# Optimization experiments

Measured on AMD Instinct MI355X. Metric: run time of the kernel, lower is better.

Reference implementation:

```python
import jax, jax.numpy as jnp
import numpy as np

N = 10000      # nodes
E = 65536      # edges
IN = 16        # in_channels
H = 64         # hidden_channels
ED = 4         # edge_attr_dim
MLP_H = 64     # hidden width of edge-weight MLPs


def _glorot(key, shape):
    fan_in, fan_out = shape[0], shape[1]
    lim = np.sqrt(6.0 / (fan_in + fan_out)).astype(np.float32)
    return jax.random.uniform(key, shape, jnp.float32, -lim, lim)


def setup_inputs() -> dict:
    key = jax.random.key(0)
    ks = jax.random.split(key, 16)
    x = jax.random.normal(ks[0], (N, IN), dtype=jnp.float32)
    edge_index = jax.random.randint(ks[1], (2, E), 0, N, dtype=jnp.int64)
    edge_attr = jax.random.normal(ks[2], (E, ED), dtype=jnp.float32)
    return {
        "x": x,
        "edge_index": edge_index,
        "edge_attr": edge_attr,
        # nn1: Linear(ED,64) -> ReLU -> Linear(64, IN*H)
        "nn1_w1": _glorot(ks[3], (ED, MLP_H)), "nn1_b1": jnp.zeros((MLP_H,), jnp.float32),
        "nn1_w2": _glorot(ks[4], (MLP_H, IN * H)), "nn1_b2": jnp.zeros((IN * H,), jnp.float32),
        "root1": _glorot(ks[5], (IN, H)), "bias1": jnp.zeros((H,), jnp.float32),
        # nn2: Linear(ED,64) -> ReLU -> Linear(64, H*H)
        "nn2_w1": _glorot(ks[6], (ED, MLP_H)), "nn2_b1": jnp.zeros((MLP_H,), jnp.float32),
        "nn2_w2": _glorot(ks[7], (MLP_H, H * H)), "nn2_b2": jnp.zeros((H * H,), jnp.float32),
        "root2": _glorot(ks[8], (H, H)), "bias2": jnp.zeros((H,), jnp.float32),
        # readout MLP
        "lin1_w": _glorot(ks[9], (H, 8)), "lin1_b": jnp.zeros((8,), jnp.float32),
        "lin2_w": _glorot(ks[10], (8, 1)), "lin2_b": jnp.zeros((1,), jnp.float32),
    }


def _nnconv(x, src, dst, edge_attr, w1, b1, w2, b2, root, bias, cin, cout):
    # Edge-conditioned weight generation: MLP(edge_attr) -> [E, cin, cout]
    h = jax.nn.relu(edge_attr @ w1 + b1)
    We = (h @ w2 + b2).reshape(-1, cin, cout)
    # Per-edge matmul: message_e = x[src_e] @ We_e  -> [E, cout]
    msg = jnp.einsum('ei,eio->eo', x[src], We)
    # Scatter mean over destination nodes
    s = jax.ops.segment_sum(msg, dst, num_segments=N)
    cnt = jax.ops.segment_sum(jnp.ones((msg.shape[0],), x.dtype), dst, num_segments=N)
    agg = s / jnp.maximum(cnt, 1.0)[:, None]
    # Root transform + bias (PyG NNConv defaults: root_weight=True, bias=True)
    return agg + x @ root + bias


def reference(x, edge_index, edge_attr,
              nn1_w1, nn1_b1, nn1_w2, nn1_b2, root1, bias1,
              nn2_w1, nn2_b1, nn2_w2, nn2_b2, root2, bias2,
              lin1_w, lin1_b, lin2_w, lin2_b):
    # Dropout layers are identity in eval mode.
    src, dst = edge_index[0], edge_index[1]
    h = jax.nn.relu(_nnconv(x, src, dst, edge_attr,
                            nn1_w1, nn1_b1, nn1_w2, nn1_b2, root1, bias1, IN, H))
    h = jax.nn.relu(_nnconv(h, src, dst, edge_attr,
                            nn2_w1, nn2_b1, nn2_w2, nn2_b2, root2, bias2, H, H))
    h = jax.nn.relu(h @ lin1_w + lin1_b)
    return (h @ lin2_w + lin2_b)[:, 0]  # squeeze(-1) -> [N]
```

## Files before the change

kernel.cpp:

```cpp
#include <hip/hip_runtime.h>
#include <hip/hip_bf16.h>

#define NN 10000
#define EE 65536

using short8  = __attribute__((ext_vector_type(8))) short;
using float4v = __attribute__((ext_vector_type(4))) float;

__device__ __forceinline__ unsigned short f2b(float f){
  union { float f; unsigned int u; } v; v.f = f;
  unsigned int u = v.u;
  unsigned int r = (u + 0x7fff + ((u >> 16) & 1)) >> 16;
  return (unsigned short)r;
}


__global__ void k_hist(const int* __restrict__ dst, int* __restrict__ cnt){
  int e = blockIdx.x*256 + threadIdx.x;
  if(e < EE) atomicAdd(&cnt[dst[e]], 1);
}

__global__ __launch_bounds__(1024) void k_scan(const int* __restrict__ cnt, int* __restrict__ offs, int* __restrict__ cursor){
  const int T = 1024, PER = (NN + T - 1)/T;
  int tid = threadIdx.x;
  int base = tid*PER;
  int local[PER];
  int s = 0;
  #pragma unroll
  for(int j=0;j<PER;j++){
    int i = base+j;
    int v = (i<NN)? cnt[i] : 0;
    local[j] = s;
    s += v;
  }
  int lane = tid & 63, wv = tid >> 6;
  int val = s;
  #pragma unroll
  for(int o=1;o<64;o<<=1){
    int u = __shfl_up(val, o, 64);
    if(lane >= o) val += u;
  }
  __shared__ int wsum[16];
  if(lane==63) wsum[wv] = val;
  __syncthreads();
  if(tid==0){
    int acc=0;
    #pragma unroll
    for(int i=0;i<16;i++){ int t2=wsum[i]; wsum[i]=acc; acc+=t2; }
  }
  __syncthreads();
  int thr_excl = wsum[wv] + (val - s);
  #pragma unroll
  for(int j=0;j<PER;j++){
    int i = base+j;
    if(i<NN){ int e = thr_excl + local[j]; offs[i]=e; cursor[i]=e; }
  }
  if(tid == T-1) offs[NN] = thr_excl + s;
}

__global__ void k_scatter(const int* __restrict__ dst, int* __restrict__ cursor, int* __restrict__ elist){
  int e = blockIdx.x*256 + threadIdx.x;
  if(e < EE){ int p = atomicAdd(&cursor[dst[e]], 1); elist[p] = e; }
}


__global__ void k_permB(const float* __restrict__ w2, unsigned short* __restrict__ Bt, int cin){
  int idx = blockIdx.x*256 + threadIdx.x;
  int K = cin*64;
  int total = 64*K;
  if(idx < total){
    int o = idx / K;
    int k = idx - o*K;
    int m = k / cin;
    int i = k - m*cin;
    Bt[idx] = f2b(w2[(size_t)m*(cin*64) + i*64 + o]);
  }
}


__global__ void k_edge_mlp(const float* __restrict__ ea, const float* __restrict__ w1,
                           const float* __restrict__ b1, float* __restrict__ h){
  int idx = blockIdx.x*256 + threadIdx.x;
  if(idx < EE*64){
    int m = idx & 63;
    int e = idx >> 6;
    const float* a = ea + (size_t)e*4;
    float acc = b1[m] + a[0]*w1[m] + a[1]*w1[64+m] + a[2]*w1[128+m] + a[3]*w1[192+m];
    h[idx] = fmaxf(acc, 0.f);
  }
}


__global__ __launch_bounds__(64) void k_accK1(const float* __restrict__ x, const int* __restrict__ src,
    const int* __restrict__ offs, const int* __restrict__ elist, const float* __restrict__ h,
    unsigned short* __restrict__ K1, float* __restrict__ XS, int v0){
  int v = v0 + blockIdx.x;
  int L = threadIdx.x;
  int i = L & 15, mg = L >> 4;
  __shared__ float sh[2][64];
  float acc[16];
  #pragma unroll
  for(int j=0;j<16;j++) acc[j]=0.f;
  float xs = 0.f;
  int p0 = offs[v], p1 = offs[v+1];
  float h_nxt = 0.f, x_nxt = 0.f;
  if(p0 < p1){
    int e = elist[p0];
    h_nxt = h[(size_t)e*64 + L];
    x_nxt = x[(size_t)src[e]*16 + i];
  }
  for(int p=p0;p<p1;p++){
    int buf = (p-p0)&1;
    float hv = h_nxt, xv = x_nxt;
    sh[buf][L] = hv;
    __syncthreads();
    if(p+1<p1){
      int e = elist[p+1];
      h_nxt = h[(size_t)e*64 + L];
      x_nxt = x[(size_t)src[e]*16 + i];
    }
    xs += xv;
    #pragma unroll
    for(int j4=0;j4<4;j4++){
      float4 h4 = *(float4*)&sh[buf][mg*16 + j4*4];
      acc[j4*4+0] += h4.x*xv; acc[j4*4+1] += h4.y*xv;
      acc[j4*4+2] += h4.z*xv; acc[j4*4+3] += h4.w*xv;
    }
  }
  unsigned short* Kv = K1 + (size_t)blockIdx.x*1024;
  #pragma unroll
  for(int j=0;j<16;j++) Kv[(mg*16+j)*16 + i] = f2b(acc[j]);
  if(mg==0) XS[(size_t)v*64 + i] = xs;
}


__global__ __launch_bounds__(64) void k_accK2(const float* __restrict__ x1, const int* __restrict__ src,
    const int* __restrict__ offs, const int* __restrict__ elist, const float* __restrict__ h,
    unsigned short* __restrict__ K, float* __restrict__ XS, int v0){
  int v = v0 + blockIdx.x;
  int L = threadIdx.x;
  __shared__ float sh[2][64];
  float acc[64];
  #pragma unroll
  for(int m=0;m<64;m++) acc[m]=0.f;
  float xs = 0.f;
  int p0 = offs[v], p1 = offs[v+1];
  float h_nxt = 0.f, x_nxt = 0.f;
  if(p0 < p1){
    int e = elist[p0];
    h_nxt = h[(size_t)e*64 + L];
    x_nxt = x1[(size_t)src[e]*64 + L];
  }
  for(int p=p0;p<p1;p++){
    int buf = (p-p0)&1;
    float hv = h_nxt, xv = x_nxt;
    sh[buf][L] = hv;
    __syncthreads();
    if(p+1<p1){
      int e = elist[p+1];
      h_nxt = h[(size_t)e*64 + L];
      x_nxt = x1[(size_t)src[e]*64 + L];
    }
    xs += xv;
    #pragma unroll
    for(int m4=0;m4<16;m4++){
      float4 h4 = *(float4*)&sh[buf][m4*4];
      acc[m4*4+0] += h4.x*xv; acc[m4*4+1] += h4.y*xv;
      acc[m4*4+2] += h4.z*xv; acc[m4*4+3] += h4.w*xv;
    }
  }
  unsigned short* Kv = K + (size_t)blockIdx.x*4096;
  #pragma unroll
  for(int m=0;m<64;m++) Kv[m*64 + L] = f2b(acc[m]);
  XS[(size_t)v*64 + L] = xs;
}


#define GBK 64

__global__ __launch_bounds__(256) void k_gemm(const unsigned short* __restrict__ A,
    const unsigned short* __restrict__ Bt, float* __restrict__ P,
    int rows, int Ktot, int Kc){
  __shared__ unsigned short As[128*72];
  __shared__ unsigned short Bs[64*72];
  int t = threadIdx.x;
  int lane = t & 63;
  int w = t >> 6;
  int row0 = blockIdx.x*128;
  int k0 = blockIdx.y*Kc;

  int srow  = t >> 3;
  int skseg = (t & 7) << 3;

  float4v acc[2][4];
  #pragma unroll
  for(int rt=0;rt<2;rt++)
    #pragma unroll
    for(int ct=0;ct<4;ct++)
      #pragma unroll
      for(int q=0;q<4;q++) acc[rt][ct][q]=0.f;

  int lrow = lane & 15;
  int lk   = (lane >> 4) << 3;

  for(int kk=0; kk<Kc; kk+=GBK){
    __syncthreads();
    #pragma unroll
    for(int q=0;q<4;q++){
      int r = srow + 32*q;
      int gr = row0 + r;
      short8 val = {0,0,0,0,0,0,0,0};
      if(gr < rows) val = *(const short8*)(A + (size_t)gr*Ktot + k0 + kk + skseg);
      *(short8*)(As + r*72 + skseg) = val;
    }
    #pragma unroll
    for(int q=0;q<2;q++){
      int o = srow + 32*q;
      *(short8*)(Bs + o*72 + skseg) = *(const short8*)(Bt + (size_t)o*Ktot + k0 + kk + skseg);
    }
    __syncthreads();
    #pragma unroll
    for(int k32=0;k32<2;k32++){
      int kf = k32*32 + lk;
      short8 a0 = *(short8*)(As + (w*32      + lrow)*72 + kf);
      short8 a1 = *(short8*)(As + (w*32 + 16 + lrow)*72 + kf);
      #pragma unroll
      for(int ct=0;ct<4;ct++){
        short8 b = *(short8*)(Bs + (ct*16 + lrow)*72 + kf);
        acc[0][ct] = __builtin_amdgcn_mfma_f32_16x16x32_bf16(a0, b, acc[0][ct], 0,0,0);
        acc[1][ct] = __builtin_amdgcn_mfma_f32_16x16x32_bf16(a1, b, acc[1][ct], 0,0,0);
      }
    }
  }
  size_t base = (size_t)blockIdx.y*rows*64;
  int quad = lane >> 4;
  #pragma unroll
  for(int rt=0;rt<2;rt++){
    #pragma unroll
    for(int ct=0;ct<4;ct++){
      int c = ct*16 + lrow;
      #pragma unroll
      for(int reg=0;reg<4;reg++){
        int r = row0 + w*32 + rt*16 + quad*4 + reg;
        if(r < rows) P[base + (size_t)r*64 + c] = acc[rt][ct][reg];
      }
    }
  }
}


template<int CIN, int SPLIT>
__global__ __launch_bounds__(256) void k_reduce_ep(const float* __restrict__ P, int rows, int v0,
    const float* __restrict__ XS, const float* __restrict__ b2, const float* __restrict__ xprev,
    const float* __restrict__ root, const float* __restrict__ bias, const int* __restrict__ offs,
    float* __restrict__ out){
  int idx = blockIdx.x*256 + threadIdx.x;
  if(idx >= rows*16) return;
  int r = idx >> 4, og = (idx & 15) << 2;
  int v = v0 + r;

  float4 s = make_float4(0.f,0.f,0.f,0.f);
  #pragma unroll
  for(int z=0; z<SPLIT; z++){
    float4 p = *(const float4*)(P + ((size_t)z*rows + r)*64 + og);
    s.x += p.x; s.y += p.y; s.z += p.z; s.w += p.w;
  }
  #pragma unroll
  for(int i=0;i<CIN;i++){
    float xsv = XS[(size_t)v*64 + i];
    float4 b = *(const float4*)(b2 + i*64 + og);
    s.x += xsv*b.x; s.y += xsv*b.y; s.z += xsv*b.z; s.w += xsv*b.w;
  }
  float4 rt = make_float4(0.f,0.f,0.f,0.f);
  #pragma unroll
  for(int i=0;i<CIN;i++){
    float xv = xprev[(size_t)v*CIN + i];
    float4 wv = *(const float4*)(root + i*64 + og);
    rt.x += xv*wv.x; rt.y += xv*wv.y; rt.z += xv*wv.z; rt.w += xv*wv.w;
  }
  float c = (float)(offs[v+1]-offs[v]); c = fmaxf(c, 1.f);
  float inv = 1.f/c;
  float4 bi = *(const float4*)(bias + og);
  float4 o;
  o.x = fmaxf(s.x*inv + rt.x + bi.x, 0.f);
  o.y = fmaxf(s.y*inv + rt.y + bi.y, 0.f);
  o.z = fmaxf(s.z*inv + rt.z + bi.z, 0.f);
  o.w = fmaxf(s.w*inv + rt.w + bi.w, 0.f);
  *(float4*)(out + (size_t)v*64 + og) = o;
}


__global__ void k_readout(const float* __restrict__ x2, const float* __restrict__ lw1,
                          const float* __restrict__ lb1, const float* __restrict__ lw2,
                          const float* __restrict__ lb2, float* __restrict__ out){
  int v = blockIdx.x*256 + threadIdx.x;
  if(v >= NN) return;
  float accj[8];
  #pragma unroll
  for(int j=0;j<8;j++) accj[j] = lb1[j];
  const float* xr = x2 + (size_t)v*64;
  #pragma unroll 16
  for(int i=0;i<64;i++){
    float xv = xr[i];
    #pragma unroll
    for(int j=0;j<8;j++) accj[j] += xv*lw1[i*8+j];
  }
  float o = lb2[0];
  #pragma unroll
  for(int j=0;j<8;j++) o += fmaxf(accj[j],0.f)*lw2[j];
  out[v] = o;
}


extern "C" void kernel_launch(void* const* d_in, const int* in_sizes, int n_in,
                              void* d_out, int out_size, void* d_ws, size_t ws_size,
                              hipStream_t stream) {
  const float* x      = (const float*)d_in[0];
  const int*   ei     = (const int*)d_in[1];
  const float* ea     = (const float*)d_in[2];
  const float* nn1_w1 = (const float*)d_in[3];
  const float* nn1_b1 = (const float*)d_in[4];
  const float* nn1_w2 = (const float*)d_in[5];
  const float* nn1_b2 = (const float*)d_in[6];
  const float* root1  = (const float*)d_in[7];
  const float* bias1  = (const float*)d_in[8];
  const float* nn2_w1 = (const float*)d_in[9];
  const float* nn2_b1 = (const float*)d_in[10];
  const float* nn2_w2 = (const float*)d_in[11];
  const float* nn2_b2 = (const float*)d_in[12];
  const float* root2  = (const float*)d_in[13];
  const float* bias2  = (const float*)d_in[14];
  const float* lin1_w = (const float*)d_in[15];
  const float* lin1_b = (const float*)d_in[16];
  const float* lin2_w = (const float*)d_in[17];
  const float* lin2_b = (const float*)d_in[18];
  float* out = (float*)d_out;

  const int* srcIdx = ei;
  const int* dstIdx = ei + EE;

  char* w = (char*)d_ws;
  size_t off = 0;
  auto alloc = [&](size_t bytes)->void*{
    void* p = w + off;
    off = (off + bytes + 255) & ~(size_t)255;
    return p;
  };
  int*            cnt    = (int*)           alloc((size_t)NN*4);
  int*            offs   = (int*)           alloc((size_t)(NN+1)*4);
  int*            cursor = (int*)           alloc((size_t)NN*4);
  int*            elist  = (int*)           alloc((size_t)EE*4);
  float*          h      = (float*)         alloc((size_t)EE*64*4);
  float*          XS     = (float*)         alloc((size_t)NN*64*4);
  float*          x1     = (float*)         alloc((size_t)NN*64*4);
  float*          x2b    = (float*)         alloc((size_t)NN*64*4);
  unsigned short* Bp     = (unsigned short*)alloc((size_t)4096*64*2);
  size_t fixedBytes = off;
  size_t R = (ws_size > fixedBytes) ? (ws_size - fixedBytes) : 0;

  const int S1 = 8, S2 = 16;
  long long C2max = (long long)(R / (4096*2 + S2*64*4));
  long long C1max = (long long)(R / (1024*2 + S1*64*4));
  if(C2max > NN) C2max = NN;
  if(C1max > NN) C1max = NN;
  if(C2max < 128) C2max = 128;
  if(C1max < 128) C1max = 128;
  int nch2 = (int)((NN + C2max - 1)/C2max);
  int nch1 = (int)((NN + C1max - 1)/C1max);
  long long C2 = (NN + nch2 - 1)/nch2;
  long long C1 = (NN + nch1 - 1)/nch1;

  unsigned short* Kbuf = (unsigned short*)(w + off);

  hipMemsetAsync(cnt, 0, (size_t)NN*4, stream);
  k_hist   <<<(EE+255)/256, 256, 0, stream>>>(dstIdx, cnt);
  k_scan   <<<1, 1024, 0, stream>>>(cnt, offs, cursor);
  k_scatter<<<(EE+255)/256, 256, 0, stream>>>(dstIdx, cursor, elist);

  k_permB   <<<(64*16*64+255)/256, 256, 0, stream>>>(nn1_w2, Bp, 16);
  k_edge_mlp<<<(EE*64+255)/256, 256, 0, stream>>>(ea, nn1_w1, nn1_b1, h);
  {
    float* P = (float*)(w + off + (size_t)C1*1024*2);
    for(long long v0=0; v0<NN; v0+=C1){
      int rows = (int)((NN - v0 < C1) ? (NN - v0) : C1);
      k_accK1<<<rows, 64, 0, stream>>>(x, srcIdx, offs, elist, h, Kbuf, XS, (int)v0);
      dim3 g((rows+127)/128, S1);
      k_gemm<<<g, 256, 0, stream>>>(Kbuf, Bp, P, rows, 1024, 1024/S1);
      k_reduce_ep<16,S1><<<(rows*16+255)/256, 256, 0, stream>>>(P, rows, (int)v0, XS, nn1_b2, x,
                                                                 root1, bias1, offs, x1);
    }
  }

  k_permB   <<<(64*64*64+255)/256, 256, 0, stream>>>(nn2_w2, Bp, 64);
  k_edge_mlp<<<(EE*64+255)/256, 256, 0, stream>>>(ea, nn2_w1, nn2_b1, h);
  {
    float* P = (float*)(w + off + (size_t)C2*4096*2);
    for(long long v0=0; v0<NN; v0+=C2){
      int rows = (int)((NN - v0 < C2) ? (NN - v0) : C2);
      k_accK2<<<rows, 64, 0, stream>>>(x1, srcIdx, offs, elist, h, Kbuf, XS, (int)v0);
      dim3 g((rows+127)/128, S2);
      k_gemm<<<g, 256, 0, stream>>>(Kbuf, Bp, P, rows, 4096, 4096/S2);
      k_reduce_ep<64,S2><<<(rows*16+255)/256, 256, 0, stream>>>(P, rows, (int)v0, XS, nn2_b2, x1,
                                                                 root2, bias2, offs, x2b);
    }
  }

  k_readout<<<(NN+255)/256, 256, 0, stream>>>(x2b, lin1_w, lin1_b, lin2_w, lin2_b, out);
}
```

Measured before the change: 240.1 us.

## Fuse prep kernels, single-pass layers, vectorize accK2, fuse readout into reduce

Merges count-zeroing, both weight permutations and both edge MLPs into one prep launch with separate h and B buffers per layer. Adds a single-chunk path that runs each layer as one accK/gemm/reduce sequence over all nodes when the workspace is large enough. Lowers the split-K factors. Rewrites accK2 so each thread takes a float4 of x and a 16-wide slice of h, writing vector stores, and fuses the readout MLP into the layer-2 reduce epilogue. In exchange it uses more workspace and adds a second code path.

```diff
diff --git a/kernel.cpp b/kernel.cpp
--- a/kernel.cpp
+++ b/kernel.cpp
@@ -12,6 +12,49 @@
   unsigned int u = v.u;
   unsigned int r = (u + 0x7fff + ((u >> 16) & 1)) >> 16;
   return (unsigned short)r;
+}
+
+
+__device__ __forceinline__ void do_permB(int idx, const float* __restrict__ w2,
+                                         unsigned short* __restrict__ Bt, int cin){
+  int K = cin*64;
+  int o = idx / K;
+  int k = idx - o*K;
+  int m = k / cin;
+  int i = k - m*cin;
+  Bt[idx] = f2b(w2[(size_t)m*(cin*64) + i*64 + o]);
+}
+
+__device__ __forceinline__ void do_mlp(int idx, const float* __restrict__ ea,
+                                       const float* __restrict__ w1, const float* __restrict__ b1,
+                                       float* __restrict__ h){
+  int m = idx & 63;
+  int e = idx >> 6;
+  const float* a = ea + (size_t)e*4;
+  float acc = b1[m] + a[0]*w1[m] + a[1]*w1[64+m] + a[2]*w1[128+m] + a[3]*w1[192+m];
+  h[idx] = fmaxf(acc, 0.f);
+}
+
+__global__ __launch_bounds__(256) void k_prep(const float* __restrict__ ea,
+    const float* __restrict__ w1a, const float* __restrict__ b1a, float* __restrict__ h1,
+    const float* __restrict__ w1b, const float* __restrict__ b1b, float* __restrict__ h2,
+    const float* __restrict__ w2a, unsigned short* __restrict__ Bt1,
+    const float* __restrict__ w2b, unsigned short* __restrict__ Bt2,
+    int* __restrict__ cnt){
+  int b = blockIdx.x;
+  int t = threadIdx.x;
+  if(b < 40){
+    int i = b*256 + t;
+    if(i < NN) cnt[i] = 0;
+  } else if(b < 296){
+    do_permB((b-40)*256 + t, w2a, Bt1, 16);
+  } else if(b < 1320){
+    do_permB((b-296)*256 + t, w2b, Bt2, 64);
+  } else if(b < 17704){
+    do_mlp((b-1320)*256 + t, ea, w1a, b1a, h1);
+  } else {
+    do_mlp((b-17704)*256 + t, ea, w1b, b1b, h2);
+  }
 }
 
 
@@ -61,33 +104,6 @@
 __global__ void k_scatter(const int* __restrict__ dst, int* __restrict__ cursor, int* __restrict__ elist){
   int e = blockIdx.x*256 + threadIdx.x;
   if(e < EE){ int p = atomicAdd(&cursor[dst[e]], 1); elist[p] = e; }
-}
-
-
-__global__ void k_permB(const float* __restrict__ w2, unsigned short* __restrict__ Bt, int cin){
-  int idx = blockIdx.x*256 + threadIdx.x;
-  int K = cin*64;
-  int total = 64*K;
-  if(idx < total){
-    int o = idx / K;
-    int k = idx - o*K;
-    int m = k / cin;
-    int i = k - m*cin;
-    Bt[idx] = f2b(w2[(size_t)m*(cin*64) + i*64 + o]);
-  }
-}
-
-
-__global__ void k_edge_mlp(const float* __restrict__ ea, const float* __restrict__ w1,
-                           const float* __restrict__ b1, float* __restrict__ h){
-  int idx = blockIdx.x*256 + threadIdx.x;
-  if(idx < EE*64){
-    int m = idx & 63;
-    int e = idx >> 6;
-    const float* a = ea + (size_t)e*4;
-    float acc = b1[m] + a[0]*w1[m] + a[1]*w1[64+m] + a[2]*w1[128+m] + a[3]*w1[192+m];
-    h[idx] = fmaxf(acc, 0.f);
-  }
 }
 
 
@@ -139,40 +155,53 @@
     unsigned short* __restrict__ K, float* __restrict__ XS, int v0){
   int v = v0 + blockIdx.x;
   int L = threadIdx.x;
+  int q = L & 15, mg = L >> 4;
+  int i0 = q << 2;
   __shared__ float sh[2][64];
-  float acc[64];
-  #pragma unroll
-  for(int m=0;m<64;m++) acc[m]=0.f;
-  float xs = 0.f;
+  float acc[16][4];
+  #pragma unroll
+  for(int j=0;j<16;j++)
+    #pragma unroll
+    for(int c=0;c<4;c++) acc[j][c]=0.f;
+  float4 xs = make_float4(0.f,0.f,0.f,0.f);
   int p0 = offs[v], p1 = offs[v+1];
-  float h_nxt = 0.f, x_nxt = 0.f;
+  float h_nxt = 0.f;
+  float4 x_nxt = make_float4(0.f,0.f,0.f,0.f);
   if(p0 < p1){
     int e = elist[p0];
     h_nxt = h[(size_t)e*64 + L];
-    x_nxt = x1[(size_t)src[e]*64 + L];
+    x_nxt = *(const float4*)(x1 + (size_t)src[e]*64 + i0);
   }
   for(int p=p0;p<p1;p++){
     int buf = (p-p0)&1;
-    float hv = h_nxt, xv = x_nxt;
-    sh[buf][L] = hv;
+    float4 xv = x_nxt;
+    sh[buf][L] = h_nxt;
     __syncthreads();
     if(p+1<p1){
       int e = elist[p+1];
       h_nxt = h[(size_t)e*64 + L];
-      x_nxt = x1[(size_t)src[e]*64 + L];
-    }
-    xs += xv;
-    #pragma unroll
-    for(int m4=0;m4<16;m4++){
-      float4 h4 = *(float4*)&sh[buf][m4*4];
-      acc[m4*4+0] += h4.x*xv; acc[m4*4+1] += h4.y*xv;
-      acc[m4*4+2] += h4.z*xv; acc[m4*4+3] += h4.w*xv;
+      x_nxt = *(const float4*)(x1 + (size_t)src[e]*64 + i0);
+    }
+    xs.x += xv.x; xs.y += xv.y; xs.z += xv.z; xs.w += xv.w;
+    #pragma unroll
+    for(int j4=0;j4<4;j4++){
+      float4 h4 = *(float4*)&sh[buf][mg*16 + j4*4];
+      #pragma unroll
+      for(int tq=0;tq<4;tq++){
+        float hv = (tq==0)?h4.x:(tq==1)?h4.y:(tq==2)?h4.z:h4.w;
+        acc[j4*4+tq][0] += hv*xv.x; acc[j4*4+tq][1] += hv*xv.y;
+        acc[j4*4+tq][2] += hv*xv.z; acc[j4*4+tq][3] += hv*xv.w;
+      }
     }
   }
   unsigned short* Kv = K + (size_t)blockIdx.x*4096;
   #pragma unroll
-  for(int m=0;m<64;m++) Kv[m*64 + L] = f2b(acc[m]);
-  XS[(size_t)v*64 + L] = xs;
+  for(int j=0;j<16;j++){
+    ushort4 u;
+    u.x = f2b(acc[j][0]); u.y = f2b(acc[j][1]); u.z = f2b(acc[j][2]); u.w = f2b(acc[j][3]);
+    *(ushort4*)(Kv + (mg*16+j)*64 + i0) = u;
+  }
+  if(mg==0) *(float4*)(XS + (size_t)v*64 + i0) = xs;
 }
 
 
@@ -198,7 +227,7 @@
     #pragma unroll
     for(int ct=0;ct<4;ct++)
       #pragma unroll
-      for(int q=0;q<4;q++) acc[rt][ct][q]=0.f;
+      for(int qq=0;qq<4;qq++) acc[rt][ct][qq]=0.f;
 
   int lrow = lane & 15;
   int lk   = (lane >> 4) << 3;
@@ -206,16 +235,16 @@
   for(int kk=0; kk<Kc; kk+=GBK){
     __syncthreads();
     #pragma unroll
-    for(int q=0;q<4;q++){
-      int r = srow + 32*q;
+    for(int qq=0;qq<4;qq++){
+      int r = srow + 32*qq;
       int gr = row0 + r;
       short8 val = {0,0,0,0,0,0,0,0};
       if(gr < rows) val = *(const short8*)(A + (size_t)gr*Ktot + k0 + kk + skseg);
       *(short8*)(As + r*72 + skseg) = val;
     }
     #pragma unroll
-    for(int q=0;q<2;q++){
-      int o = srow + 32*q;
+    for(int qq=0;qq<2;qq++){
+      int o = srow + 32*qq;
       *(short8*)(Bs + o*72 + skseg) = *(const short8*)(Bt + (size_t)o*Ktot + k0 + kk + skseg);
     }
     __syncthreads();
@@ -287,6 +316,72 @@
   o.z = fmaxf(s.z*inv + rt.z + bi.z, 0.f);
   o.w = fmaxf(s.w*inv + rt.w + bi.w, 0.f);
   *(float4*)(out + (size_t)v*64 + og) = o;
+}
+
+
+template<int SPLIT>
+__global__ __launch_bounds__(256) void k_red2_ro(const float* __restrict__ P, int rows,
+    const float* __restrict__ XS, const float* __restrict__ b2, const float* __restrict__ x1,
+    const float* __restrict__ root, const float* __restrict__ bias, const int* __restrict__ offs,
+    const float* __restrict__ lw1, const float* __restrict__ lb1,
+    const float* __restrict__ lw2, const float* __restrict__ lb2,
+    float* __restrict__ out){
+  __shared__ float row[16][68];
+  __shared__ float hjs[16][8];
+  int tid = threadIdx.x;
+  int idx = blockIdx.x*256 + tid;
+  int r = idx >> 4, og = (idx & 15) << 2;
+  int n = tid >> 4;
+  int nbase = blockIdx.x*16;
+  int ninblk = rows - nbase; if(ninblk > 16) ninblk = 16;
+
+  float4 o = make_float4(0.f,0.f,0.f,0.f);
+  if(r < rows){
+    float4 s = make_float4(0.f,0.f,0.f,0.f);
+    #pragma unroll
+    for(int z=0; z<SPLIT; z++){
+      float4 p = *(const float4*)(P + ((size_t)z*rows + r)*64 + og);
+      s.x += p.x; s.y += p.y; s.z += p.z; s.w += p.w;
+    }
+    #pragma unroll
+    for(int i=0;i<64;i++){
+      float xsv = XS[(size_t)r*64 + i];
+      float4 b = *(const float4*)(b2 + i*64 + og);
+      s.x += xsv*b.x; s.y += xsv*b.y; s.z += xsv*b.z; s.w += xsv*b.w;
+    }
+    float4 rt = make_float4(0.f,0.f,0.f,0.f);
+    #pragma unroll
+    for(int i=0;i<64;i++){
+      float xv = x1[(size_t)r*64 + i];
+      float4 wv = *(const float4*)(root + i*64 + og);
+      rt.x += xv*wv.x; rt.y += xv*wv.y; rt.z += xv*wv.z; rt.w += xv*wv.w;
+    }
+    float c = (float)(offs[r+1]-offs[r]); c = fmaxf(c, 1.f);
+    float inv = 1.f/c;
+    float4 bi = *(const float4*)(bias + og);
+    o.x = fmaxf(s.x*inv + rt.x + bi.x, 0.f);
+    o.y = fmaxf(s.y*inv + rt.y + bi.y, 0.f);
+    o.z = fmaxf(s.z*inv + rt.z + bi.z, 0.f);
+    o.w = fmaxf(s.w*inv + rt.w + bi.w, 0.f);
+  }
+  *(float4*)&row[n][og] = o;
+  __syncthreads();
+  if(tid < 128){
+    int n2 = tid >> 3, j = tid & 7;
+    if(n2 < ninblk){
+      float a = lb1[j];
+      #pragma unroll
+      for(int i=0;i<64;i++) a += row[n2][i]*lw1[i*8+j];
+      hjs[n2][j] = fmaxf(a, 0.f)*lw2[j];
+    }
+  }
+  __syncthreads();
+  if(tid < 16 && tid < ninblk){
+    float s = lb2[0];
+    #pragma unroll
+    for(int j=0;j<8;j++) s += hjs[tid][j];
+    out[nbase + tid] = s;
+  }
 }
 
 
@@ -350,60 +445,73 @@
   int*            offs   = (int*)           alloc((size_t)(NN+1)*4);
   int*            cursor = (int*)           alloc((size_t)NN*4);
   int*            elist  = (int*)           alloc((size_t)EE*4);
-  float*          h      = (float*)         alloc((size_t)EE*64*4);
+  float*          h1     = (float*)         alloc((size_t)EE*64*4);
+  float*          h2     = (float*)         alloc((size_t)EE*64*4);
   float*          XS     = (float*)         alloc((size_t)NN*64*4);
   float*          x1     = (float*)         alloc((size_t)NN*64*4);
-  float*          x2b    = (float*)         alloc((size_t)NN*64*4);
-  unsigned short* Bp     = (unsigned short*)alloc((size_t)4096*64*2);
+  unsigned short* Bt1    = (unsigned short*)alloc((size_t)64*1024*2);
+  unsigned short* Bt2    = (unsigned short*)alloc((size_t)64*4096*2);
   size_t fixedBytes = off;
   size_t R = (ws_size > fixedBytes) ? (ws_size - fixedBytes) : 0;
 
-  const int S1 = 8, S2 = 16;
-  long long C2max = (long long)(R / (4096*2 + S2*64*4));
-  long long C1max = (long long)(R / (1024*2 + S1*64*4));
-  if(C2max > NN) C2max = NN;
-  if(C1max > NN) C1max = NN;
-  if(C2max < 128) C2max = 128;
-  if(C1max < 128) C1max = 128;
-  int nch2 = (int)((NN + C2max - 1)/C2max);
-  int nch1 = (int)((NN + C1max - 1)/C1max);
-  long long C2 = (NN + nch2 - 1)/nch2;
-  long long C1 = (NN + nch1 - 1)/nch1;
-
-  unsigned short* Kbuf = (unsigned short*)(w + off);
-
-  hipMemsetAsync(cnt, 0, (size_t)NN*4, stream);
+  const int S1 = 4, S2 = 8;
+  size_t needSingle = (size_t)NN*4096*2 + (size_t)S2*NN*64*4;
+  bool single = (R >= needSingle + 4096);
+
+  k_prep<<<34088, 256, 0, stream>>>(ea, nn1_w1, nn1_b1, h1, nn2_w1, nn2_b1, h2,
+                                    nn1_w2, Bt1, nn2_w2, Bt2, cnt);
   k_hist   <<<(EE+255)/256, 256, 0, stream>>>(dstIdx, cnt);
   k_scan   <<<1, 1024, 0, stream>>>(cnt, offs, cursor);
   k_scatter<<<(EE+255)/256, 256, 0, stream>>>(dstIdx, cursor, elist);
 
-  k_permB   <<<(64*16*64+255)/256, 256, 0, stream>>>(nn1_w2, Bp, 16);
-  k_edge_mlp<<<(EE*64+255)/256, 256, 0, stream>>>(ea, nn1_w1, nn1_b1, h);
-  {
-    float* P = (float*)(w + off + (size_t)C1*1024*2);
-    for(long long v0=0; v0<NN; v0+=C1){
-      int rows = (int)((NN - v0 < C1) ? (NN - v0) : C1);
-      k_accK1<<<rows, 64, 0, stream>>>(x, srcIdx, offs, elist, h, Kbuf, XS, (int)v0);
-      dim3 g((rows+127)/128, S1);
-      k_gemm<<<g, 256, 0, stream>>>(Kbuf, Bp, P, rows, 1024, 1024/S1);
-      k_reduce_ep<16,S1><<<(rows*16+255)/256, 256, 0, stream>>>(P, rows, (int)v0, XS, nn1_b2, x,
-                                                                 root1, bias1, offs, x1);
-    }
-  }
-
-  k_permB   <<<(64*64*64+255)/256, 256, 0, stream>>>(nn2_w2, Bp, 64);
-  k_edge_mlp<<<(EE*64+255)/256, 256, 0, stream>>>(ea, nn2_w1, nn2_b1, h);
-  {
-    float* P = (float*)(w + off + (size_t)C2*4096*2);
-    for(long long v0=0; v0<NN; v0+=C2){
-      int rows = (int)((NN - v0 < C2) ? (NN - v0) : C2);
-      k_accK2<<<rows, 64, 0, stream>>>(x1, srcIdx, offs, elist, h, Kbuf, XS, (int)v0);
-      dim3 g((rows+127)/128, S2);
-      k_gemm<<<g, 256, 0, stream>>>(Kbuf, Bp, P, rows, 4096, 4096/S2);
-      k_reduce_ep<64,S2><<<(rows*16+255)/256, 256, 0, stream>>>(P, rows, (int)v0, XS, nn2_b2, x1,
-                                                                 root2, bias2, offs, x2b);
-    }
-  }
-
-  k_readout<<<(NN+255)/256, 256, 0, stream>>>(x2b, lin1_w, lin1_b, lin2_w, lin2_b, out);
-}
+  if(single){
+    unsigned short* Kbuf = (unsigned short*)(w + off);
+    float* P = (float*)(w + off + (size_t)NN*4096*2);
+
+    k_accK1<<<NN, 64, 0, stream>>>(x, srcIdx, offs, elist, h1, Kbuf, XS, 0);
+    {
+      dim3 g((NN+127)/128, S1);
+      k_gemm<<<g, 256, 0, stream>>>(Kbuf, Bt1, P, NN, 1024, 1024/S1);
+    }
+    k_reduce_ep<16,S1><<<(NN*16+255)/256, 256, 0, stream>>>(P, NN, 0, XS, nn1_b2, x,
+                                                             root1, bias1, offs, x1);
+    k_accK2<<<NN, 64, 0, stream>>>(x1, srcIdx, offs, elist, h2, Kbuf, XS, 0);
+    {
+      dim3 g((NN+127)/128, S2);
+      k_gemm<<<g, 256, 0, stream>>>(Kbuf, Bt2, P, NN, 4096, 4096/S2);
+    }
+    k_red2_ro<S2><<<(NN+15)/16, 256, 0, stream>>>(P, NN, XS, nn2_b2, x1, root2, bias2, offs,
+                                                   lin1_w, lin1_b, lin2_w, lin2_b, out);
+  } else {
+    float* x2b = (float*)alloc((size_t)NN*64*4);
+    R = (ws_size > off) ? (ws_size - off) : 0;
+    long long C2 = (long long)(R / (4096*2 + S2*64*4));
+    long long C1 = (long long)(R / (1024*2 + S1*64*4));
+    if(C2 > NN) C2 = NN; if(C1 > NN) C1 = NN;
+    if(C2 < 128) C2 = 128; if(C1 < 128) C1 = 128;
+    unsigned short* Kbuf = (unsigned short*)(w + off);
+    {
+      float* P = (float*)(w + off + (size_t)C1*1024*2);
+      for(long long v0=0; v0<NN; v0+=C1){
+        int rows = (int)((NN - v0 < C1) ? (NN - v0) : C1);
+        k_accK1<<<rows, 64, 0, stream>>>(x, srcIdx, offs, elist, h1, Kbuf, XS, (int)v0);
+        dim3 g((rows+127)/128, S1);
+        k_gemm<<<g, 256, 0, stream>>>(Kbuf, Bt1, P, rows, 1024, 1024/S1);
+        k_reduce_ep<16,S1><<<(rows*16+255)/256, 256, 0, stream>>>(P, rows, (int)v0, XS, nn1_b2, x,
+                                                                   root1, bias1, offs, x1);
+      }
+    }
+    {
+      float* P = (float*)(w + off + (size_t)C2*4096*2);
+      for(long long v0=0; v0<NN; v0+=C2){
+        int rows = (int)((NN - v0 < C2) ? (NN - v0) : C2);
+        k_accK2<<<rows, 64, 0, stream>>>(x1, srcIdx, offs, elist, h2, Kbuf, XS, (int)v0);
+        dim3 g((rows+127)/128, S2);
+        k_gemm<<<g, 256, 0, stream>>>(Kbuf, Bt2, P, rows, 4096, 4096/S2);
+        k_reduce_ep<64,S2><<<(rows*16+255)/256, 256, 0, stream>>>(P, rows, (int)v0, XS, nn2_b2, x1,
+                                                                   root2, bias2, offs, x2b);
+      }
+    }
+    k_readout<<<(NN+255)/256, 256, 0, stream>>>(x2b, lin1_w, lin1_b, lin2_w, lin2_b, out);
+  }
+}
```

Result: faster. 226.3 us (-5.7%).
